# Performance work log

Hardware: AMD Instinct MI355X
Metric: run time of the kernel (lower is better)

The kernel has to match this reference:

```python
import jax, jax.numpy as jnp
import numpy as np

VOCAB, D = 32000, 1024
EPS = 1e-5

def setup_inputs() -> dict:
    key = jax.random.key(0)
    k1, k2, k3, k4 = jax.random.split(key, 4)
    patch_embeddings = jax.random.normal(k1, (16, 256, D), dtype=jnp.float32)
    text_prototypes = jax.random.normal(k2, (VOCAB, D), dtype=jnp.float32) * 0.02
    # nn.Linear(d, d): weight [d, d], bias [d]
    lim = 1.0 / np.sqrt(D)
    W = jax.random.uniform(k3, (D, D), minval=-lim, maxval=lim, dtype=jnp.float32)
    b = jax.random.uniform(k4, (D,), minval=-lim, maxval=lim, dtype=jnp.float32)
    gamma = jnp.ones((D,), dtype=jnp.float32)
    beta = jnp.zeros((D,), dtype=jnp.float32)
    return {"patch_embeddings": patch_embeddings, "text_prototypes": text_prototypes,
            "W": W, "b": b, "gamma": gamma, "beta": beta}

def _layer_norm(x, gamma, beta):
    mu = jnp.mean(x, axis=-1, keepdims=True)
    var = jnp.mean(jnp.square(x - mu), axis=-1, keepdims=True)
    return (x - mu) * jax.lax.rsqrt(var + EPS) * gamma + beta

def reference(patch_embeddings, text_prototypes, W, b, gamma, beta):
    # similarities: [B, P, V]
    sims = jnp.einsum('bpd,vd->bpv', patch_embeddings, text_prototypes)
    attn = jax.nn.softmax(sims, axis=-1)
    reprogrammed = jnp.einsum('bpv,vd->bpd', attn, text_prototypes)
    transformed = jnp.einsum('bpd,ed->bpe', reprogrammed, W) + b
    return _layer_norm(patch_embeddings + transformed, gamma, beta)
```

## Files before the change

kernel.cpp:

```cpp
#include <hip/hip_runtime.h>
#include <hip/hip_bf16.h>
#include <cstdint>
#include <cstddef>

#define D_DIM 1024
#define VOCAB 32000
#define ROWS  4096

typedef __attribute__((ext_vector_type(8))) short bf16x8;
typedef __attribute__((ext_vector_type(4))) float f32x4;
typedef __attribute__((ext_vector_type(4))) int   i32x4;
typedef __attribute__((ext_vector_type(8))) int   i32x8;

static __device__ __forceinline__ i32x8 cat8(i32x4 lo, i32x4 hi) {
  return __builtin_shufflevector(lo, hi, 0, 1, 2, 3, 4, 5, 6, 7);
}

static __device__ __forceinline__ unsigned short f2bf(float f) {
  union { float f; unsigned int u; } c; c.f = f;
  unsigned int u = c.u;
  u += 0x7fffu + ((u >> 16) & 1u);
  return (unsigned short)(u >> 16);
}

static __device__ __forceinline__ int pk8(float a, float b) {
  return __builtin_amdgcn_cvt_pk_fp8_f32(a, b, 0, false);
}

static __device__ __forceinline__ void gload_lds16(const void* g, void* s) {
  __builtin_amdgcn_global_load_lds(
      (const __attribute__((address_space(1))) uint32_t*)(g),
      (__attribute__((address_space(3))) uint32_t*)(s), 16, 0, 0);
}

__global__ void k_cvt(const float* __restrict__ src, short* __restrict__ dst, int n4) {
  int i = blockIdx.x * 256 + threadIdx.x;
  if (i < n4) {
    float4 v = *(const float4*)(src + (size_t)i * 4);
    ushort4 u;
    u.x = f2bf(v.x); u.y = f2bf(v.y); u.z = f2bf(v.z); u.w = f2bf(v.w);
    *(ushort4*)(dst + (size_t)i * 4) = u;
  }
}

__global__ void k_cvt_q8(const float* __restrict__ src, uint8_t* __restrict__ dst) {
  int i = blockIdx.x * 256 + threadIdx.x;
  float4 a = *(const float4*)(src + (size_t)i * 8);
  float4 b = *(const float4*)(src + (size_t)i * 8 + 4);
  uint2 o;
  o.x = (pk8(a.x, a.y) & 0xffff) | (pk8(a.z, a.w) << 16);
  o.y = (pk8(b.x, b.y) & 0xffff) | (pk8(b.z, b.w) << 16);
  *(uint2*)(dst + (size_t)i * 8) = o;
}

__global__ void k_prep_K8(const float* __restrict__ src, uint8_t* __restrict__ kb,
                          uint8_t* __restrict__ kt, int R, int C) {
  __shared__ uint8_t tile[64][68];
  int t  = threadIdx.x;
  int r0 = blockIdx.x * 64;
  int c0 = blockIdx.y * 64;
  int lr = t >> 4;
  int lc = (t & 15) * 4;
#pragma unroll
  for (int i = 0; i < 4; ++i) {
    int r = lr + 16 * i;
    float4 v = *(const float4*)(src + (size_t)(r0 + r) * C + c0 + lc);
    unsigned p = (pk8(v.x * 64.f, v.y * 64.f) & 0xffff) | (pk8(v.z * 64.f, v.w * 64.f) << 16);
    *(unsigned*)&tile[r][lc] = p;
    *(unsigned*)(kb + (size_t)(r0 + r) * C + c0 + lc) = p;
  }
  __syncthreads();
#pragma unroll
  for (int i = 0; i < 4; ++i) {
    int c = lr + 16 * i;
    unsigned p = tile[lc + 0][c] | (tile[lc + 1][c] << 8) |
                 (tile[lc + 2][c] << 16) | ((unsigned)tile[lc + 3][c] << 24);
    *(unsigned*)(kt + (size_t)(c0 + c) * R + r0 + lc) = p;
  }
}

#define PS8 144
__global__ __launch_bounds__(256) void k_gemm8(
    const uint8_t* __restrict__ A, int lda,
    const uint8_t* __restrict__ B, int ldb,
    int Kdim, int mode,
    uint8_t* __restrict__ Pout, long ldp, float* __restrict__ den,
    float* __restrict__ Cacc)
{
  __shared__ uint8_t smem[32768];
  uint8_t* As = smem;
  uint8_t* Bs = smem + 16384;

  int tid  = threadIdx.x;
  int wave = tid >> 6;
  int lane = tid & 63;
  int quad = lane >> 4;
  int t16  = lane & 15;
  int wy = wave >> 1, wx = wave & 1;

  long mBase, nBase;
  if (mode == 0) { mBase = (long)blockIdx.x * 128; nBase = (long)blockIdx.y * 128; }
  else           { mBase = (long)blockIdx.y * 128; nBase = (long)blockIdx.x * 128; }
  int k0 = blockIdx.z * Kdim;

  const uint8_t* Ab = A + (size_t)mBase * lda + k0;
  const uint8_t* Bb = B + (size_t)nBase * ldb + k0;
  int lrow = lane >> 3;
  int lcol = ((lane & 7) ^ lrow) * 16;

  f32x4 acc[4][4];
#pragma unroll
  for (int i = 0; i < 4; ++i)
#pragma unroll
    for (int j = 0; j < 4; ++j) acc[i][j] = (f32x4){0.f, 0.f, 0.f, 0.f};

  int sw = t16 & 7;
  int co0 = (((quad << 1) ^ sw) << 4);
  const int SC1 = 0x7F7F7F7F;

  for (int kk = 0; kk < Kdim; kk += 128) {
#pragma unroll
    for (int i = 0; i < 4; ++i) {
      int row = wave * 32 + i * 8;
      gload_lds16(Ab + (size_t)(row + lrow) * lda + kk + lcol, &As[row * 128]);
      gload_lds16(Bb + (size_t)(row + lrow) * ldb + kk + lcol, &Bs[row * 128]);
    }
    __syncthreads();
    i32x8 af[4], bfr[4];
#pragma unroll
    for (int mi = 0; mi < 4; ++mi) {
      const uint8_t* rp = &As[(wy * 64 + mi * 16 + t16) * 128];
      af[mi] = cat8(*(const i32x4*)(rp + co0), *(const i32x4*)(rp + (co0 ^ 16)));
    }
#pragma unroll
    for (int ni = 0; ni < 4; ++ni) {
      const uint8_t* rp = &Bs[(wx * 64 + ni * 16 + t16) * 128];
      bfr[ni] = cat8(*(const i32x4*)(rp + co0), *(const i32x4*)(rp + (co0 ^ 16)));
    }
#pragma unroll
    for (int mi = 0; mi < 4; ++mi)
#pragma unroll
      for (int ni = 0; ni < 4; ++ni)
        acc[mi][ni] = __builtin_amdgcn_mfma_scale_f32_16x16x128_f8f6f4(
            af[mi], bfr[ni], acc[mi][ni], 0, 0, 0, SC1, 0, SC1);
    __syncthreads();
  }

  if (mode == 0) {
    float rsum[4][4];
#pragma unroll
    for (int mi = 0; mi < 4; ++mi)
#pragma unroll
      for (int r = 0; r < 4; ++r) rsum[mi][r] = 0.f;
#pragma unroll
    for (int mi = 0; mi < 4; ++mi) {
      int rloc = wy * 64 + mi * 16 + quad * 4;
#pragma unroll
      for (int ni = 0; ni < 4; ++ni) {
        int cloc = wx * 64 + ni * 16 + t16;
#pragma unroll
        for (int r = 0; r < 4; ++r) {
          float e = __expf(acc[mi][ni][r] * 0.015625f);
          smem[(rloc + r) * PS8 + cloc] = (uint8_t)pk8(e, e);
          rsum[mi][r] += e;
        }
      }
    }
#pragma unroll
    for (int mi = 0; mi < 4; ++mi)
#pragma unroll
      for (int r = 0; r < 4; ++r) {
        float s = rsum[mi][r];
        s += __shfl_xor(s, 1);
        s += __shfl_xor(s, 2);
        s += __shfl_xor(s, 4);
        s += __shfl_xor(s, 8);
        if (t16 == 0)
          atomicAdd(&den[mBase + wy * 64 + mi * 16 + quad * 4 + r], s);
      }
    __syncthreads();
    int rr  = tid >> 3;
    int c16 = (tid & 7) * 16;
#pragma unroll
    for (int i = 0; i < 4; ++i) {
      int row = i * 32 + rr;
      i32x4 v = *(const i32x4*)&smem[row * PS8 + c16];
      __builtin_nontemporal_store(v, (i32x4*)&Pout[(size_t)(mBase + row) * ldp + nBase + c16]);
    }
  } else {
#pragma unroll
    for (int mi = 0; mi < 4; ++mi) {
      long row = mBase + wy * 64 + mi * 16 + quad * 4;
#pragma unroll
      for (int ni = 0; ni < 4; ++ni) {
        long col = nBase + wx * 64 + ni * 16 + t16;
#pragma unroll
        for (int r = 0; r < 4; ++r)
          atomicAdd(&Cacc[(size_t)(row + r) * 1024 + col], acc[mi][ni][r]);
      }
    }
  }
}

#define G2NT 125
__global__ __launch_bounds__(512, 2) void k_g2(
    const uint8_t* __restrict__ P, const uint8_t* __restrict__ KT,
    float* __restrict__ n0, float* __restrict__ n1)
{
  __shared__ uint8_t smem[98304];

  int tid  = threadIdx.x;
  int wave = tid >> 6;
  int lane = tid & 63;
  int quad = lane >> 4;
  int t16  = lane & 15;
  int wm = wave >> 2;
  int wn = wave & 3;

  int xn = blockIdx.x & 3;
  int zz = (blockIdx.x >> 2) & 1;
  int ym = blockIdx.x >> 3;
  long mBase = (long)ym * 128;
  long nBase = (long)xn * 256;
  int  k0    = zz * 16000;

  const uint8_t* Ab = P  + (size_t)mBase * VOCAB + k0;
  const uint8_t* Bb = KT + (size_t)nBase * VOCAB + k0;
  int lrow = lane >> 3;
  int lcol = ((lane & 7) ^ lrow) * 16;

  f32x4 acc[4][4];
#pragma unroll
  for (int i = 0; i < 4; ++i)
#pragma unroll
    for (int j = 0; j < 4; ++j) acc[i][j] = (f32x4){0.f, 0.f, 0.f, 0.f};

  int sw  = t16 & 7;
  int co0 = (((quad << 1) ^ sw) << 4);
  const int SC1 = 0x7F7F7F7F;

  auto STAGE = [&](int slot, int t) {
    uint8_t* As = &smem[slot * 49152];
    uint8_t* Bs = As + 16384;
    long kk = (long)t * 128;
#pragma unroll
    for (int g = 0; g < 2; ++g) {
      int r0 = wave * 16 + g * 8;
      gload_lds16(Ab + (size_t)(r0 + lrow) * VOCAB + kk + lcol, As + r0 * 128);
    }
#pragma unroll
    for (int g = 0; g < 4; ++g) {
      int r0 = wave * 32 + g * 8;
      gload_lds16(Bb + (size_t)(r0 + lrow) * VOCAB + kk + lcol, Bs + r0 * 128);
    }
  };

  STAGE(0, 0);
  STAGE(1, 1);

  for (int t = 0; t < G2NT; ++t) {
    const uint8_t* As = &smem[(t & 1) * 49152];
    const uint8_t* Bs = As + 16384;

    if (t + 1 < G2NT)
      asm volatile("s_waitcnt vmcnt(6)\n\ts_barrier" ::: "memory");
    else
      asm volatile("s_waitcnt vmcnt(0)\n\ts_barrier" ::: "memory");

    i32x8 af[4], bfr[4];
#pragma unroll
    for (int mi = 0; mi < 4; ++mi) {
      const uint8_t* rp = As + (wm * 64 + mi * 16 + t16) * 128;
      af[mi] = cat8(*(const i32x4*)(rp + co0), *(const i32x4*)(rp + (co0 ^ 16)));
    }
#pragma unroll
    for (int ni = 0; ni < 4; ++ni) {
      const uint8_t* rp = Bs + (wn * 64 + ni * 16 + t16) * 128;
      bfr[ni] = cat8(*(const i32x4*)(rp + co0), *(const i32x4*)(rp + (co0 ^ 16)));
    }
    __builtin_amdgcn_s_setprio(1);
#pragma unroll
    for (int mi = 0; mi < 4; ++mi)
#pragma unroll
      for (int ni = 0; ni < 4; ++ni)
        acc[mi][ni] = __builtin_amdgcn_mfma_scale_f32_16x16x128_f8f6f4(
            af[mi], bfr[ni], acc[mi][ni], 0, 0, 0, SC1, 0, SC1);
    __builtin_amdgcn_s_setprio(0);
    asm volatile("s_barrier" ::: "memory");
    if (t + 2 < G2NT) STAGE(t & 1, t + 2);
  }

  float* outp = zz ? n1 : n0;
#pragma unroll
  for (int mi = 0; mi < 4; ++mi) {
    long row = mBase + wm * 64 + mi * 16 + quad * 4;
#pragma unroll
    for (int ni = 0; ni < 4; ++ni) {
      long col = nBase + wn * 64 + ni * 16 + t16;
#pragma unroll
      for (int r = 0; r < 4; ++r)
        __builtin_nontemporal_store(acc[mi][ni][r],
                                    &outp[(size_t)(row + r) * D_DIM + col]);
    }
  }
}

__global__ __launch_bounds__(256) void k_gemm_bf(
    const short* __restrict__ A, int lda,
    const short* __restrict__ B, int ldb, int Kdim,
    const float* __restrict__ bias, const float* __restrict__ resid,
    float* __restrict__ Cout)
{
  __shared__ short smem[16384];
  short* As = smem;
  short* Bs = smem + 8192;

  int tid  = threadIdx.x;
  int wave = tid >> 6;
  int lane = tid & 63;
  int quad = lane >> 4;
  int t16  = lane & 15;
  int wy = wave >> 1, wx = wave & 1;

  long mBase = (long)blockIdx.y * 128;
  long nBase = (long)blockIdx.x * 128;

  const short* Ab = A + (size_t)mBase * lda;
  const short* Bb = B + (size_t)nBase * ldb;
  int lrow = lane >> 3;
  int lcol = ((lane & 7) ^ lrow) * 8;

  f32x4 acc[4][4];
#pragma unroll
  for (int i = 0; i < 4; ++i)
#pragma unroll
    for (int j = 0; j < 4; ++j) acc[i][j] = (f32x4){0.f, 0.f, 0.f, 0.f};

  int sw = t16 & 7;

  for (int kk = 0; kk < Kdim; kk += 64) {
#pragma unroll
    for (int i = 0; i < 4; ++i) {
      int row = wave * 32 + i * 8;
      gload_lds16(Ab + (size_t)(row + lrow) * lda + kk + lcol, &As[row * 64]);
      gload_lds16(Bb + (size_t)(row + lrow) * ldb + kk + lcol, &Bs[row * 64]);
    }
    __syncthreads();
#pragma unroll
    for (int kc = 0; kc < 8; kc += 4) {
      bf16x8 af[4], bfr[4];
#pragma unroll
      for (int mi = 0; mi < 4; ++mi)
        af[mi] = *(const bf16x8*)&As[(wy * 64 + mi * 16 + t16) * 64 +
                                     (((kc + quad) ^ sw) << 3)];
#pragma unroll
      for (int ni = 0; ni < 4; ++ni)
        bfr[ni] = *(const bf16x8*)&Bs[(wx * 64 + ni * 16 + t16) * 64 +
                                      (((kc + quad) ^ sw) << 3)];
#pragma unroll
      for (int mi = 0; mi < 4; ++mi)
#pragma unroll
        for (int ni = 0; ni < 4; ++ni)
          acc[mi][ni] = __builtin_amdgcn_mfma_f32_16x16x32_bf16(af[mi], bfr[ni],
                                                                acc[mi][ni], 0, 0, 0);
    }
    __syncthreads();
  }

#pragma unroll
  for (int mi = 0; mi < 4; ++mi) {
    long row = mBase + wy * 64 + mi * 16 + quad * 4;
#pragma unroll
    for (int ni = 0; ni < 4; ++ni) {
      long col = nBase + wx * 64 + ni * 16 + t16;
#pragma unroll
      for (int r = 0; r < 4; ++r) {
        size_t idx = (size_t)(row + r) * 1024 + col;
        Cout[idx] = acc[mi][ni][r] + bias[col] + resid[idx];
      }
    }
  }
}

__global__ void k_div(const float* __restrict__ n0, const float* __restrict__ n1,
                      const float* __restrict__ den, short* __restrict__ out) {
  int i = (blockIdx.x * 256 + threadIdx.x) * 4;
  float4 a = *(const float4*)(n0 + i);
  float4 b = *(const float4*)(n1 + i);
  float inv = 0.015625f / den[i >> 10];
  ushort4 u;
  u.x = f2bf((a.x + b.x) * inv); u.y = f2bf((a.y + b.y) * inv);
  u.z = f2bf((a.z + b.z) * inv); u.w = f2bf((a.w + b.w) * inv);
  *(ushort4*)(out + i) = u;
}

__global__ __launch_bounds__(256) void k_ln(const float* __restrict__ x,
                                            const float* __restrict__ gamma,
                                            const float* __restrict__ beta,
                                            float* __restrict__ out) {
  __shared__ float s_sum[4], s_sq[4];
  int row = blockIdx.x;
  int tid = threadIdx.x;
  const float* xr = x + (size_t)row * 1024;
  float4 v = *(const float4*)(xr + tid * 4);
  float s = v.x + v.y + v.z + v.w;
  float q = v.x * v.x + v.y * v.y + v.z * v.z + v.w * v.w;
#pragma unroll
  for (int off = 32; off >= 1; off >>= 1) {
    s += __shfl_down(s, off);
    q += __shfl_down(q, off);
  }
  int wv = tid >> 6;
  if ((tid & 63) == 0) { s_sum[wv] = s; s_sq[wv] = q; }
  __syncthreads();
  float tot  = s_sum[0] + s_sum[1] + s_sum[2] + s_sum[3];
  float totq = s_sq[0] + s_sq[1] + s_sq[2] + s_sq[3];
  float mu   = tot * (1.0f / 1024.0f);
  float var  = totq * (1.0f / 1024.0f) - mu * mu;
  float rstd = rsqrtf(var + 1e-5f);
  float4 g = *(const float4*)(gamma + tid * 4);
  float4 b = *(const float4*)(beta + tid * 4);
  float4 o;
  o.x = (v.x - mu) * rstd * g.x + b.x;
  o.y = (v.y - mu) * rstd * g.y + b.y;
  o.z = (v.z - mu) * rstd * g.z + b.z;
  o.w = (v.w - mu) * rstd * g.w + b.w;
  *(float4*)(out + (size_t)row * 1024 + tid * 4) = o;
}

extern "C" void kernel_launch(void* const* d_in, const int* in_sizes, int n_in,
                              void* d_out, int out_size, void* d_ws, size_t ws_size,
                              hipStream_t stream) {
  const float* patch = (const float*)d_in[0];
  const float* proto = (const float*)d_in[1];
  const float* W     = (const float*)d_in[2];
  const float* bvec  = (const float*)d_in[3];
  const float* gamma = (const float*)d_in[4];
  const float* beta  = (const float*)d_in[5];
  float* out = (float*)d_out;

  char* ws = (char*)d_ws;
  size_t off = 0;
  uint8_t* Q8  = (uint8_t*)(ws + off); off += (size_t)ROWS * D_DIM;
  uint8_t* Kb8 = (uint8_t*)(ws + off); off += (size_t)VOCAB * D_DIM;
  uint8_t* KT8 = (uint8_t*)(ws + off); off += (size_t)VOCAB * D_DIM;
  short*   Wb  = (short*)(ws + off);   off += (size_t)D_DIM * D_DIM * 2;
  short*   Rb  = (short*)(ws + off);   off += (size_t)ROWS * D_DIM * 2;
  uint8_t* P8  = (uint8_t*)(ws + off); off += (size_t)ROWS * VOCAB;
  float*   num = (float*)(ws + off);   off += (size_t)ROWS * D_DIM * 4;
  float*   den = (float*)(ws + off);   off += (size_t)ROWS * 4;
  float*   pre = (float*)P8;
  float*   nz0 = (float*)Kb8;
  float*   nz1 = num;

  hipMemsetAsync(den, 0, ROWS * sizeof(float), stream);

  k_cvt_q8<<<ROWS * D_DIM / 8 / 256, 256, 0, stream>>>(patch, Q8);
  k_cvt<<<D_DIM * D_DIM / 4 / 256, 256, 0, stream>>>(W, Wb, D_DIM * D_DIM / 4);
  k_prep_K8<<<dim3(VOCAB / 64, D_DIM / 64), 256, 0, stream>>>(proto, Kb8, KT8, VOCAB, D_DIM);

  k_gemm8<<<dim3(ROWS / 128, VOCAB / 128, 1), 256, 0, stream>>>(
      Q8, D_DIM, Kb8, D_DIM, D_DIM, 0,
      P8, (long)VOCAB, den, nullptr);

  k_g2<<<256, 512, 0, stream>>>(P8, KT8, nz0, nz1);

  k_div<<<ROWS * D_DIM / 4 / 256, 256, 0, stream>>>(nz0, nz1, den, Rb);

  k_gemm_bf<<<dim3(D_DIM / 128, ROWS / 128), 256, 0, stream>>>(
      Rb, D_DIM, Wb, D_DIM, D_DIM, bvec, patch, pre);

  k_ln<<<ROWS, 256, 0, stream>>>(pre, gamma, beta, out);
}
```

Before: 646.8 us.

## Double-buffer the FP8 similarity GEMM and swizzle its block order

Replaces the generic k_gemm8 (mode 0) with a specialized k_g1 that double-buffers A/B tiles in 64KB LDS. It waits with s_waitcnt vmcnt plus raw barriers so the next K-slab's loads overlap the MFMAs, and raises wave priority around the MFMA block. It also remaps the 1D grid with a swizzle so consecutive blocks share tiles for better L2 reuse, and drops the nontemporal hint on the P store. The larger LDS footprint limits occupancy to about two blocks per CU, and the hand-written waitcnt counts depend on the exact number of outstanding loads per stage.

```diff
diff --git a/kernel.cpp b/kernel.cpp
--- a/kernel.cpp
+++ b/kernel.cpp
@@ -80,16 +80,13 @@
 }
 
 #define PS8 144
-__global__ __launch_bounds__(256) void k_gemm8(
-    const uint8_t* __restrict__ A, int lda,
-    const uint8_t* __restrict__ B, int ldb,
-    int Kdim, int mode,
-    uint8_t* __restrict__ Pout, long ldp, float* __restrict__ den,
-    float* __restrict__ Cacc)
+#define G1NT 8
+__global__ __launch_bounds__(256, 2) void k_g1(
+    const uint8_t* __restrict__ A,
+    const uint8_t* __restrict__ B,
+    uint8_t* __restrict__ Pout, float* __restrict__ den)
 {
-  __shared__ uint8_t smem[32768];
-  uint8_t* As = smem;
-  uint8_t* Bs = smem + 16384;
+  __shared__ uint8_t smem[65536];
 
   int tid  = threadIdx.x;
   int wave = tid >> 6;
@@ -98,13 +95,14 @@
   int t16  = lane & 15;
   int wy = wave >> 1, wx = wave & 1;
 
-  long mBase, nBase;
-  if (mode == 0) { mBase = (long)blockIdx.x * 128; nBase = (long)blockIdx.y * 128; }
-  else           { mBase = (long)blockIdx.y * 128; nBase = (long)blockIdx.x * 128; }
-  int k0 = blockIdx.z * Kdim;
-
-  const uint8_t* Ab = A + (size_t)mBase * lda + k0;
-  const uint8_t* Bb = B + (size_t)nBase * ldb + k0;
+  int swz = (blockIdx.x & 7) * 1000 + (blockIdx.x >> 3);
+  int nt  = swz >> 5;
+  int mt  = swz & 31;
+  long mBase = (long)mt * 128;
+  long nBase = (long)nt * 128;
+
+  const uint8_t* Ab = A + (size_t)mBase * D_DIM;
+  const uint8_t* Bb = B + (size_t)nBase * D_DIM;
   int lrow = lane >> 3;
   int lcol = ((lane & 7) ^ lrow) * 16;
 
@@ -114,18 +112,34 @@
 #pragma unroll
     for (int j = 0; j < 4; ++j) acc[i][j] = (f32x4){0.f, 0.f, 0.f, 0.f};
 
-  int sw = t16 & 7;
+  int sw  = t16 & 7;
   int co0 = (((quad << 1) ^ sw) << 4);
   const int SC1 = 0x7F7F7F7F;
 
-  for (int kk = 0; kk < Kdim; kk += 128) {
+  auto STAGE = [&](int slot, int t) {
+    uint8_t* As = &smem[slot * 32768];
+    uint8_t* Bs = As + 16384;
+    int kk = t * 128;
 #pragma unroll
     for (int i = 0; i < 4; ++i) {
       int row = wave * 32 + i * 8;
-      gload_lds16(Ab + (size_t)(row + lrow) * lda + kk + lcol, &As[row * 128]);
-      gload_lds16(Bb + (size_t)(row + lrow) * ldb + kk + lcol, &Bs[row * 128]);
-    }
-    __syncthreads();
+      gload_lds16(Ab + (size_t)(row + lrow) * D_DIM + kk + lcol, As + row * 128);
+      gload_lds16(Bb + (size_t)(row + lrow) * D_DIM + kk + lcol, Bs + row * 128);
+    }
+  };
+
+  STAGE(0, 0);
+  STAGE(1, 1);
+
+  for (int t = 0; t < G1NT; ++t) {
+    const uint8_t* As = &smem[(t & 1) * 32768];
+    const uint8_t* Bs = As + 16384;
+
+    if (t + 1 < G1NT)
+      asm volatile("s_waitcnt vmcnt(8)\n\ts_barrier" ::: "memory");
+    else
+      asm volatile("s_waitcnt vmcnt(0)\n\ts_barrier" ::: "memory");
+
     i32x8 af[4], bfr[4];
 #pragma unroll
     for (int mi = 0; mi < 4; ++mi) {
@@ -137,68 +151,57 @@
       const uint8_t* rp = &Bs[(wx * 64 + ni * 16 + t16) * 128];
       bfr[ni] = cat8(*(const i32x4*)(rp + co0), *(const i32x4*)(rp + (co0 ^ 16)));
     }
+    __builtin_amdgcn_s_setprio(1);
 #pragma unroll
     for (int mi = 0; mi < 4; ++mi)
 #pragma unroll
       for (int ni = 0; ni < 4; ++ni)
         acc[mi][ni] = __builtin_amdgcn_mfma_scale_f32_16x16x128_f8f6f4(
             af[mi], bfr[ni], acc[mi][ni], 0, 0, 0, SC1, 0, SC1);
-    __syncthreads();
-  }
-
-  if (mode == 0) {
-    float rsum[4][4];
-#pragma unroll
-    for (int mi = 0; mi < 4; ++mi)
-#pragma unroll
-      for (int r = 0; r < 4; ++r) rsum[mi][r] = 0.f;
-#pragma unroll
-    for (int mi = 0; mi < 4; ++mi) {
-      int rloc = wy * 64 + mi * 16 + quad * 4;
-#pragma unroll
-      for (int ni = 0; ni < 4; ++ni) {
-        int cloc = wx * 64 + ni * 16 + t16;
-#pragma unroll
-        for (int r = 0; r < 4; ++r) {
-          float e = __expf(acc[mi][ni][r] * 0.015625f);
-          smem[(rloc + r) * PS8 + cloc] = (uint8_t)pk8(e, e);
-          rsum[mi][r] += e;
-        }
+    __builtin_amdgcn_s_setprio(0);
+    asm volatile("s_barrier" ::: "memory");
+    if (t + 2 < G1NT) STAGE(t & 1, t + 2);
+  }
+
+  float rsum[4][4];
+#pragma unroll
+  for (int mi = 0; mi < 4; ++mi)
+#pragma unroll
+    for (int r = 0; r < 4; ++r) rsum[mi][r] = 0.f;
+#pragma unroll
+  for (int mi = 0; mi < 4; ++mi) {
+    int rloc = wy * 64 + mi * 16 + quad * 4;
+#pragma unroll
+    for (int ni = 0; ni < 4; ++ni) {
+      int cloc = wx * 64 + ni * 16 + t16;
+#pragma unroll
+      for (int r = 0; r < 4; ++r) {
+        float e = __expf(acc[mi][ni][r] * 0.015625f);
+        smem[(rloc + r) * PS8 + cloc] = (uint8_t)pk8(e, e);
+        rsum[mi][r] += e;
       }
     }
-#pragma unroll
-    for (int mi = 0; mi < 4; ++mi)
-#pragma unroll
-      for (int r = 0; r < 4; ++r) {
-        float s = rsum[mi][r];
-        s += __shfl_xor(s, 1);
-        s += __shfl_xor(s, 2);
-        s += __shfl_xor(s, 4);
-        s += __shfl_xor(s, 8);
-        if (t16 == 0)
-          atomicAdd(&den[mBase + wy * 64 + mi * 16 + quad * 4 + r], s);
-      }
-    __syncthreads();
-    int rr  = tid >> 3;
-    int c16 = (tid & 7) * 16;
-#pragma unroll
-    for (int i = 0; i < 4; ++i) {
-      int row = i * 32 + rr;
-      i32x4 v = *(const i32x4*)&smem[row * PS8 + c16];
-      __builtin_nontemporal_store(v, (i32x4*)&Pout[(size_t)(mBase + row) * ldp + nBase + c16]);
-    }
-  } else {
-#pragma unroll
-    for (int mi = 0; mi < 4; ++mi) {
-      long row = mBase + wy * 64 + mi * 16 + quad * 4;
-#pragma unroll
-      for (int ni = 0; ni < 4; ++ni) {
-        long col = nBase + wx * 64 + ni * 16 + t16;
-#pragma unroll
-        for (int r = 0; r < 4; ++r)
-          atomicAdd(&Cacc[(size_t)(row + r) * 1024 + col], acc[mi][ni][r]);
-      }
-    }
+  }
+#pragma unroll
+  for (int mi = 0; mi < 4; ++mi)
+#pragma unroll
+    for (int r = 0; r < 4; ++r) {
+      float s = rsum[mi][r];
+      s += __shfl_xor(s, 1);
+      s += __shfl_xor(s, 2);
+      s += __shfl_xor(s, 4);
+      s += __shfl_xor(s, 8);
+      if (t16 == 0)
+        atomicAdd(&den[mBase + wy * 64 + mi * 16 + quad * 4 + r], s);
+    }
+  __syncthreads();
+  int rr  = tid >> 3;
+  int c16 = (tid & 7) * 16;
+#pragma unroll
+  for (int i = 0; i < 4; ++i) {
+    int row = i * 32 + rr;
+    i32x4 v = *(const i32x4*)&smem[row * PS8 + c16];
+    *(i32x4*)&Pout[(size_t)(mBase + row) * VOCAB + nBase + c16] = v;
   }
 }
 
@@ -459,9 +462,7 @@
   k_cvt<<<D_DIM * D_DIM / 4 / 256, 256, 0, stream>>>(W, Wb, D_DIM * D_DIM / 4);
   k_prep_K8<<<dim3(VOCAB / 64, D_DIM / 64), 256, 0, stream>>>(proto, Kb8, KT8, VOCAB, D_DIM);
 
-  k_gemm8<<<dim3(ROWS / 128, VOCAB / 128, 1), 256, 0, stream>>>(
-      Q8, D_DIM, Kb8, D_DIM, D_DIM, 0,
-      P8, (long)VOCAB, den, nullptr);
+  k_g1<<<8000, 256, 0, stream>>>(Q8, Kb8, P8, den);
 
   k_g2<<<256, 512, 0, stream>>>(P8, KT8, nz0, nz1);
 
```

Result: no change. 647.6 us (+0.1%).
